# Performance work log

Hardware: AMD Instinct MI355X
Metric: run time of the kernel (lower is better)

Reference implementation:

```python
import jax, jax.numpy as jnp
import numpy as np

N = 50000      # nodes
E = 800000     # edges (avg degree 16)
IN = 512       # input_dim
R = 128        # feat_reduce_dim
F = 64         # hid_dim per head
H = 4          # n_heads
OUT = 64       # output_dim
ALPHA = 0.2    # leaky_relu slope


def setup_inputs() -> dict:
    key = jax.random.key(0)
    ks = jax.random.split(key, 12)
    x = jax.random.normal(ks[0], (N, IN), dtype=jnp.float32)
    edges = jax.random.randint(ks[1], (2, E), 0, N, dtype=jnp.int32)
    # per-head GAT layer params (fan-in scaled so exp(logits) stays finite)
    W_lin_h = jax.random.normal(ks[2], (H, R, IN), dtype=jnp.float32) * (IN ** -0.5)
    W_seq_h = jax.random.normal(ks[3], (H, F, R), dtype=jnp.float32) * (R ** -0.5)
    a1_h = jax.random.normal(ks[4], (H, F), dtype=jnp.float32) * (F ** -0.5)
    b1_h = jnp.zeros((H,), dtype=jnp.float32)
    a2_h = jax.random.normal(ks[5], (H, F), dtype=jnp.float32) * (F ** -0.5)
    b2_h = jnp.zeros((H,), dtype=jnp.float32)
    bias_h = jnp.zeros((H, F), dtype=jnp.float32)
    # classifier GAT layer (in = H*F = 256, out = OUT)
    W_lin_c = jax.random.normal(ks[6], (R, H * F), dtype=jnp.float32) * ((H * F) ** -0.5)
    W_seq_c = jax.random.normal(ks[7], (OUT, R), dtype=jnp.float32) * (R ** -0.5)
    a1_c = jax.random.normal(ks[8], (OUT,), dtype=jnp.float32) * (OUT ** -0.5)
    b1_c = jnp.zeros((), dtype=jnp.float32)
    a2_c = jax.random.normal(ks[9], (OUT,), dtype=jnp.float32) * (OUT ** -0.5)
    b2_c = jnp.zeros((), dtype=jnp.float32)
    bias_c = jnp.zeros((OUT,), dtype=jnp.float32)
    return dict(x=x, edges=edges, W_lin_h=W_lin_h, W_seq_h=W_seq_h, a1_h=a1_h,
                b1_h=b1_h, a2_h=a2_h, b2_h=b2_h, bias_h=bias_h,
                W_lin_c=W_lin_c, W_seq_c=W_seq_c, a1_c=a1_c, b1_c=b1_c,
                a2_c=a2_c, b2_c=b2_c, bias_c=bias_c)


def _gat_layer(x, src, dst, W_lin, W_seq, a1, b1, a2, b2, bias, concat):
    n = x.shape[0]
    h = x @ W_lin.T                    # [N, R]   (Linear, no bias)
    s = h @ W_seq.T                    # [N, F]   (Conv1d k=1 == matmul)
    f1 = s @ a1 + b1                   # [N]      (f_1 conv)
    f2 = s @ a2 + b2                   # [N]      (f_2 conv)
    logits = f1[src] + f2[dst]         # [E]  edge-gather
    coefs = jnp.exp(jax.nn.leaky_relu(logits, ALPHA))          # [E]
    denom = jax.ops.segment_sum(coefs, src, num_segments=n)    # [N]
    agg = jax.ops.segment_sum(coefs[:, None] * s[dst], src, num_segments=n)  # [N, F]
    ret = agg / denom[:, None] + bias
    return jax.nn.elu(ret) if concat else ret


def reference(x, edges, W_lin_h, W_seq_h, a1_h, b1_h, a2_h, b2_h, bias_h,
              W_lin_c, W_seq_c, a1_c, b1_c, a2_c, b2_c, bias_c):
    src, dst = edges[0], edges[1]
    # n_heads attention layers (concat=True), vmapped over the head axis
    heads = jax.vmap(
        lambda Wl, Ws, a1, b1, a2, b2, b: _gat_layer(
            x, src, dst, Wl, Ws, a1, b1, a2, b2, b, True)
    )(W_lin_h, W_seq_h, a1_h, b1_h, a2_h, b2_h, bias_h)        # [H, N, F]
    hcat = jnp.transpose(heads, (1, 0, 2)).reshape(x.shape[0], -1)  # [N, H*F]
    # classifier GAT layer (concat=False -> no ELU)
    out = _gat_layer(hcat, src, dst, W_lin_c, W_seq_c, a1_c, b1_c,
                     a2_c, b2_c, bias_c, False)                # [N, OUT]
    return out
```

## Files before the change

kernel.cpp:

```cpp
#include <hip/hip_runtime.h>
#include <hip/hip_bf16.h>
#include <cstddef>
#include <cstdint>

#define IN_DIM 512
#define R_DIM 128
#define F_DIM 64
#define H_NUM 4
#define OUT_DIM 64
#define HF 256

typedef __attribute__((ext_vector_type(4))) float f32x4;
typedef __attribute__((ext_vector_type(8))) short bf16x8;

typedef const __attribute__((address_space(1))) void gas_void;
typedef __attribute__((address_space(3))) void las_void;

__device__ __forceinline__ float bf2f(ushort u) {
    union { uint i; float f; } v; v.i = ((uint)u) << 16; return v.f;
}
__device__ __forceinline__ ushort f2bf(float f) {
    union { float f; uint i; } v; v.f = f;
    uint r = v.i + 0x7fff + ((v.i >> 16) & 1);
    return (ushort)(r >> 16);
}
__device__ __forceinline__ float u2f(uint u) {
    union { uint i; float f; } v; v.i = u; return v.f;
}

__global__ __launch_bounds__(256) void zero_i32(int* __restrict__ p, int n) {
    int i = blockIdx.x * 256 + threadIdx.x;
    if (i < n) p[i] = 0;
}

__global__ __launch_bounds__(256) void wcomb_kernel(const float* __restrict__ WlinH,
                                                    const float* __restrict__ WseqH,
                                                    const float* __restrict__ WlinC,
                                                    const float* __restrict__ WseqC,
                                                    ushort* __restrict__ Wc1,
                                                    ushort* __restrict__ Wc2) {
    int idx = blockIdx.x * 256 + threadIdx.x;
    if (idx < H_NUM * F_DIM * IN_DIM) {
        int i  = idx & (IN_DIM - 1);
        int hf = idx >> 9;
        int h  = hf >> 6;
        const float* ws = WseqH + (size_t)hf * R_DIM;
        const float* wl = WlinH + (size_t)h * R_DIM * IN_DIM + i;
        float acc = 0.0f;
#pragma unroll 8
        for (int r = 0; r < R_DIM; ++r) acc += ws[r] * wl[(size_t)r * IN_DIM];
        Wc1[idx] = f2bf(acc);
    } else {
        int idx2 = idx - H_NUM * F_DIM * IN_DIM;
        if (idx2 >= OUT_DIM * HF) return;
        int j = idx2 & (HF - 1);
        int o = idx2 >> 8;
        const float* ws = WseqC + (size_t)o * R_DIM;
        const float* wl = WlinC + j;
        float acc = 0.0f;
#pragma unroll 8
        for (int r = 0; r < R_DIM; ++r) acc += ws[r] * wl[(size_t)r * HF];
        Wc2[idx2] = f2bf(acc);
    }
}

template<int BN, int K, int FS>
__global__ __launch_bounds__(256) void gemm_f32a(const float* __restrict__ A,
                                                 const ushort* __restrict__ B,
                                                 ushort* __restrict__ C,
                                                 int M, int Ntot,
                                                 const float* __restrict__ a1,
                                                 const float* __restrict__ b1,
                                                 const float* __restrict__ a2,
                                                 const float* __restrict__ b2,
                                                 float* __restrict__ f1o,
                                                 float* __restrict__ f2o) {
    constexpr int NF = 4;
    __shared__ ushort As[32 * 64];
    __shared__ ushort Bs[BN * 64];
    const int tid = threadIdx.x;
    const int wave = tid >> 6;
    const int lane = tid & 63;
    const int lr = lane & 15;
    const int lg = lane >> 4;
    const int wr = wave & 1;
    const int wc = wave >> 1;

    const int b = blockIdx.x;
    const int by = (b >> 3) & 1;
    const int bx = (b >> 4) * 8 + (b & 7);
    const int nbx = (M + 31) >> 5;
    if (bx >= nbx) return;
    const int m0 = bx * 32;
    const int n0 = by * BN;
    const int h0 = by * 2;

    int base[2];
#pragma unroll
    for (int ks = 0; ks < 2; ++ks)
        base[ks] = lr * 128 + (((ks * 4 + lg) ^ (lr & 7)) * 16);
    const int abase0 = wr * 2048 + base[0];
    const int abase1 = wr * 2048 + base[1];

    const int s_row = tid >> 3;
    const int s_lchunk = tid & 7;
    int s_grow = m0 + s_row;
    if (s_grow >= M) s_grow = M - 1;
    const int s_ldsoff = s_row * 128 + ((s_lchunk ^ (s_row & 7)) * 16);
    const int s_goff = s_lchunk * 8;

    f32x4 acc[NF];
#pragma unroll
    for (int cb = 0; cb < NF; ++cb) acc[cb] = (f32x4)0.0f;

    for (int k0 = 0; k0 < K; k0 += 64) {
#pragma unroll
        for (int r = 0; r < BN / 32; ++r) {
            int off = r * 4096 + tid * 16;
            int row = off >> 7;
            int kch = ((off >> 4) & 7) ^ (row & 7);
            const ushort* g = B + (size_t)(n0 + row) * K + k0 + kch * 8;
            __builtin_amdgcn_global_load_lds((gas_void*)g,
                                             (las_void*)((char*)Bs + off), 16, 0, 0);
        }
        {
            const float* g = A + (size_t)s_grow * K + k0 + s_goff;
            float4 v0 = *(const float4*)(g);
            float4 v1 = *(const float4*)(g + 4);
            ushort us[8] = {f2bf(v0.x), f2bf(v0.y), f2bf(v0.z), f2bf(v0.w),
                            f2bf(v1.x), f2bf(v1.y), f2bf(v1.z), f2bf(v1.w)};
            *(uint4*)((char*)As + s_ldsoff) = *(const uint4*)us;
        }
        __syncthreads();
        {
            bf16x8 af0 = *(const bf16x8*)((const char*)As + abase0);
            bf16x8 af1 = *(const bf16x8*)((const char*)As + abase1);
            bf16x8 bfr[NF];
#pragma unroll
            for (int j = 0; j < NF; ++j)
                bfr[j] = *(const bf16x8*)((const char*)Bs + (wc * 4 + j) * 2048 + base[0]);
#pragma unroll
            for (int j = 0; j < NF; ++j)
                acc[j] = __builtin_amdgcn_mfma_f32_16x16x32_bf16(
                    af0, bfr[j], acc[j], 0, 0, 0);
#pragma unroll
            for (int j = 0; j < NF; ++j)
                bfr[j] = *(const bf16x8*)((const char*)Bs + (wc * 4 + j) * 2048 + base[1]);
#pragma unroll
            for (int j = 0; j < NF; ++j)
                acc[j] = __builtin_amdgcn_mfma_f32_16x16x32_bf16(
                    af1, bfr[j], acc[j], 0, 0, 0);
        }
        __syncthreads();
    }

    const int head = h0 + wc;
    float a1v[NF], a2v[NF];
#pragma unroll
    for (int cb = 0; cb < NF; ++cb) {
        int col = n0 + wc * 64 + cb * 16 + lr;
        a1v[cb] = a1[col];
        a2v[cb] = a2[col];
    }
    const int rowb = m0 + wr * 16 + lg * 4;
#pragma unroll
    for (int r = 0; r < 4; ++r) {
        int row = rowb + r;
        bool ok = row < M;
        float p1 = 0.f, p2 = 0.f;
#pragma unroll
        for (int cb = 0; cb < NF; ++cb) {
            float v = acc[cb][r];
            p1 += v * a1v[cb];
            p2 += v * a2v[cb];
            if (ok) C[(size_t)row * Ntot + n0 + wc * 64 + cb * 16 + lr] = f2bf(v);
        }
#pragma unroll
        for (int m = 1; m < 16; m <<= 1) {
            p1 += __shfl_xor(p1, m, 64);
            p2 += __shfl_xor(p2, m, 64);
        }
        if (lr == 0 && ok) {
            f1o[(size_t)row * FS + head] = p1 + b1[head];
            f2o[(size_t)row * FS + head] = p2 + b2[head];
        }
    }
}

template<int BN, int K, int FS>
__global__ __launch_bounds__(256) void gemm_bf16(const ushort* __restrict__ A,
                                                 const ushort* __restrict__ B,
                                                 ushort* __restrict__ C,
                                                 int M, int Ntot,
                                                 const float* __restrict__ a1,
                                                 const float* __restrict__ b1,
                                                 const float* __restrict__ a2,
                                                 const float* __restrict__ b2,
                                                 float* __restrict__ f1o,
                                                 float* __restrict__ f2o) {
    constexpr int NF = BN / 16;
    constexpr int HH = BN / 64;
    __shared__ ushort As[64 * 64];
    __shared__ ushort Bs[BN * 64];
    const int tid = threadIdx.x;
    const int wave = tid >> 6;
    const int lane = tid & 63;
    const int lr = lane & 15;
    const int lg = lane >> 4;
    const int m0 = blockIdx.x * 64;

    int base[2];
#pragma unroll
    for (int ks = 0; ks < 2; ++ks)
        base[ks] = lr * 128 + (((ks * 4 + lg) ^ (lr & 7)) * 16);
    const int abase0 = wave * 2048 + base[0];
    const int abase1 = wave * 2048 + base[1];

    f32x4 acc[NF];
#pragma unroll
    for (int cb = 0; cb < NF; ++cb) acc[cb] = (f32x4)0.0f;

    for (int k0 = 0; k0 < K; k0 += 64) {
#pragma unroll
        for (int r = 0; r < 2; ++r) {
            int off = r * 4096 + tid * 16;
            int row = off >> 7;
            int kch = ((off >> 4) & 7) ^ (row & 7);
            const ushort* g = A + (size_t)(m0 + row) * K + k0 + kch * 8;
            __builtin_amdgcn_global_load_lds((gas_void*)g,
                                             (las_void*)((char*)As + off), 16, 0, 0);
        }
#pragma unroll
        for (int r = 0; r < BN / 32; ++r) {
            int off = r * 4096 + tid * 16;
            int row = off >> 7;
            int kch = ((off >> 4) & 7) ^ (row & 7);
            const ushort* g = B + (size_t)row * K + k0 + kch * 8;
            __builtin_amdgcn_global_load_lds((gas_void*)g,
                                             (las_void*)((char*)Bs + off), 16, 0, 0);
        }
        __syncthreads();
        {
            bf16x8 af0 = *(const bf16x8*)((const char*)As + abase0);
            bf16x8 af1 = *(const bf16x8*)((const char*)As + abase1);
#pragma unroll
            for (int cg = 0; cg < NF / 4; ++cg) {
                bf16x8 bfr[4];
#pragma unroll
                for (int j = 0; j < 4; ++j)
                    bfr[j] = *(const bf16x8*)((const char*)Bs + (cg * 4 + j) * 2048 + base[0]);
#pragma unroll
                for (int j = 0; j < 4; ++j)
                    acc[cg * 4 + j] = __builtin_amdgcn_mfma_f32_16x16x32_bf16(
                        af0, bfr[j], acc[cg * 4 + j], 0, 0, 0);
#pragma unroll
                for (int j = 0; j < 4; ++j)
                    bfr[j] = *(const bf16x8*)((const char*)Bs + (cg * 4 + j) * 2048 + base[1]);
#pragma unroll
                for (int j = 0; j < 4; ++j)
                    acc[cg * 4 + j] = __builtin_amdgcn_mfma_f32_16x16x32_bf16(
                        af1, bfr[j], acc[cg * 4 + j], 0, 0, 0);
            }
        }
        __syncthreads();
    }

    float a1v[NF], a2v[NF];
#pragma unroll
    for (int cb = 0; cb < NF; ++cb) {
        int col = cb * 16 + lr;
        a1v[cb] = a1[col];
        a2v[cb] = a2[col];
    }
    const int rowb = m0 + wave * 16 + lg * 4;
#pragma unroll
    for (int r = 0; r < 4; ++r) {
        int row = rowb + r;
        bool ok = row < M;
#pragma unroll
        for (int hh = 0; hh < HH; ++hh) {
            float p1 = 0.f, p2 = 0.f;
#pragma unroll
            for (int c4 = 0; c4 < 4; ++c4) {
                int cb = hh * 4 + c4;
                float v = acc[cb][r];
                p1 += v * a1v[cb];
                p2 += v * a2v[cb];
                if (ok) C[(size_t)row * Ntot + cb * 16 + lr] = f2bf(v);
            }
#pragma unroll
            for (int m = 1; m < 16; m <<= 1) {
                p1 += __shfl_xor(p1, m, 64);
                p2 += __shfl_xor(p2, m, 64);
            }
            if (lr == 0 && ok) {
                f1o[(size_t)row * FS + hh] = p1 + b1[hh];
                f2o[(size_t)row * FS + hh] = p2 + b2[hh];
            }
        }
    }
}

__global__ __launch_bounds__(256) void hist_kernel(const int* __restrict__ src,
                                                   int* __restrict__ counts, int E) {
    int e = blockIdx.x * 256 + threadIdx.x;
    if (e < E) atomicAdd(&counts[src[e]], 1);
}

__global__ __launch_bounds__(256) void scan_blk(const int* __restrict__ counts,
                                                int* __restrict__ lexcl,
                                                int* __restrict__ part, int N) {
    __shared__ int wsum[4];
    int t = threadIdx.x;
    int g = blockIdx.x * 256 + t;
    int lane = t & 63, wid = t >> 6;
    int v = (g < N) ? counts[g] : 0;
    int x = v;
#pragma unroll
    for (int off = 1; off < 64; off <<= 1) {
        int u = __shfl_up(x, off, 64);
        if (lane >= off) x += u;
    }
    if (lane == 63) wsum[wid] = x;
    __syncthreads();
    int woff = 0;
#pragma unroll
    for (int w = 0; w < 3; ++w) if (w < wid) woff += wsum[w];
    int incl = x + woff;
    if (g < N) lexcl[g] = incl - v;
    if (t == 255) part[blockIdx.x] = incl;
}

__global__ __launch_bounds__(256) void scan_part(int* __restrict__ part, int nb) {
    __shared__ int wsum[4];
    int t = threadIdx.x;
    int lane = t & 63, wid = t >> 6;
    int v = (t < nb) ? part[t] : 0;
    int x = v;
#pragma unroll
    for (int off = 1; off < 64; off <<= 1) {
        int u = __shfl_up(x, off, 64);
        if (lane >= off) x += u;
    }
    if (lane == 63) wsum[wid] = x;
    __syncthreads();
    int woff = 0;
#pragma unroll
    for (int w = 0; w < 3; ++w) if (w < wid) woff += wsum[w];
    int incl = x + woff;
    __syncthreads();
    if (t < nb) part[t] = incl - v;
    if (t == 255) part[nb] = incl;
}

__global__ __launch_bounds__(256) void scan_add(const int* __restrict__ lexcl,
                                                const int* __restrict__ part,
                                                int* __restrict__ starts,
                                                int* __restrict__ cursor, int N, int nb) {
    int g = blockIdx.x * 256 + threadIdx.x;
    if (g < N) {
        int s = lexcl[g] + part[blockIdx.x];
        starts[g] = s;
        cursor[g] = s;
    }
    if (g == 0) starts[N] = part[nb];
}

__global__ __launch_bounds__(256) void scatter_kernel(const int* __restrict__ src,
                                                      const int* __restrict__ dst,
                                                      int* __restrict__ cursor,
                                                      int* __restrict__ dsts, int E) {
    int e = blockIdx.x * 256 + threadIdx.x;
    if (e >= E) return;
    int p = atomicAdd(&cursor[src[e]], 1);
    dsts[p] = dst[e];
}

__global__ __launch_bounds__(256) void gather1_kernel(const int* __restrict__ starts,
                                                      const int* __restrict__ dsts,
                                                      const float* __restrict__ f1,
                                                      const float* __restrict__ f2,
                                                      const ushort* __restrict__ S1,
                                                      const float* __restrict__ bias,
                                                      ushort* __restrict__ hcat, int N) {
    int n = (int)((blockIdx.x * blockDim.x + threadIdx.x) >> 6);
    int lane = threadIdx.x & 63;
    if (n >= N) return;
    const int es = lane >> 5;
    const int fl = lane & 31;
    const int head = fl >> 3;
    const float f1h = f1[(size_t)n * 4 + head];
    int beg = starts[n], end = starts[n + 1];
    float a[8] = {};
    float den = 0.f;
    int i = beg;

#define G1_EDGE(D)                                                            \
    {                                                                         \
        float g_ = f2[(size_t)(D) * 4 + head];                                \
        uint4 r_ = *(const uint4*)(S1 + (size_t)(D) * HF + fl * 8);           \
        float l_ = f1h + g_; l_ = l_ > 0.f ? l_ : 0.2f * l_;                  \
        float c_ = __expf(l_);                                                \
        a[0] += c_ * u2f(r_.x << 16);  a[1] += c_ * u2f(r_.x & 0xffff0000u);  \
        a[2] += c_ * u2f(r_.y << 16);  a[3] += c_ * u2f(r_.y & 0xffff0000u);  \
        a[4] += c_ * u2f(r_.z << 16);  a[5] += c_ * u2f(r_.z & 0xffff0000u);  \
        a[6] += c_ * u2f(r_.w << 16);  a[7] += c_ * u2f(r_.w & 0xffff0000u);  \
        den += c_;                                                            \
    }

    for (; i + 4 <= end; i += 4) {
        int dA = dsts[i + es];
        int dB = dsts[i + 2 + es];
        G1_EDGE(dA);
        G1_EDGE(dB);
    }
    if (i + 2 <= end) {
        int d = dsts[i + es];
        G1_EDGE(d);
        i += 2;
    }
    if (i < end && es == 0) {
        int d = dsts[i];
        G1_EDGE(d);
    }
#undef G1_EDGE

#pragma unroll
    for (int k = 0; k < 8; ++k) a[k] += __shfl_xor(a[k], 32, 64);
    den += __shfl_xor(den, 32, 64);

    if (es == 0) {
        float rd = __builtin_amdgcn_rcpf(den);
        float4 b0 = *(const float4*)(bias + fl * 8);
        float4 b1 = *(const float4*)(bias + fl * 8 + 4);
        float v[8];
        v[0] = a[0] * rd + b0.x; v[1] = a[1] * rd + b0.y;
        v[2] = a[2] * rd + b0.z; v[3] = a[3] * rd + b0.w;
        v[4] = a[4] * rd + b1.x; v[5] = a[5] * rd + b1.y;
        v[6] = a[6] * rd + b1.z; v[7] = a[7] * rd + b1.w;
        ushort us[8];
#pragma unroll
        for (int k = 0; k < 8; ++k) {
            float vv = v[k] > 0.f ? v[k] : __expf(v[k]) - 1.f;
            us[k] = f2bf(vv);
        }
        *(uint4*)(hcat + (size_t)n * HF + fl * 8) = *(const uint4*)us;
    }
}

__global__ __launch_bounds__(256) void gather2_kernel(const int* __restrict__ starts,
                                                      const int* __restrict__ dsts,
                                                      const float* __restrict__ f1,
                                                      const float* __restrict__ f2,
                                                      const ushort* __restrict__ S2,
                                                      const float* __restrict__ bias,
                                                      float* __restrict__ out, int N) {
    int n = (int)((blockIdx.x * blockDim.x + threadIdx.x) >> 6);
    int lane = threadIdx.x & 63;
    if (n >= N) return;
    const int es = lane >> 5;
    const int fl = lane & 31;
    const float f1u = f1[n];
    int beg = starts[n], end = starts[n + 1];
    float a0 = 0.f, a1 = 0.f, den = 0.f;
    int i = beg;

#define G2_EDGE(D)                                                            \
    {                                                                         \
        float g_ = f2[(D)];                                                   \
        uint r_ = *(const uint*)(S2 + (size_t)(D) * OUT_DIM + fl * 2);        \
        float l_ = f1u + g_; l_ = l_ > 0.f ? l_ : 0.2f * l_;                  \
        float c_ = __expf(l_);                                                \
        a0 += c_ * u2f(r_ << 16);                                             \
        a1 += c_ * u2f(r_ & 0xffff0000u);                                     \
        den += c_;                                                            \
    }

    for (; i + 4 <= end; i += 4) {
        int dA = dsts[i + es];
        int dB = dsts[i + 2 + es];
        G2_EDGE(dA);
        G2_EDGE(dB);
    }
    if (i + 2 <= end) {
        int d = dsts[i + es];
        G2_EDGE(d);
        i += 2;
    }
    if (i < end && es == 0) {
        int d = dsts[i];
        G2_EDGE(d);
    }
#undef G2_EDGE

    a0 += __shfl_xor(a0, 32, 64);
    a1 += __shfl_xor(a1, 32, 64);
    den += __shfl_xor(den, 32, 64);

    if (es == 0) {
        float rd = __builtin_amdgcn_rcpf(den);
        float2 b = *(const float2*)(bias + fl * 2);
        float2 o;
        o.x = a0 * rd + b.x;
        o.y = a1 * rd + b.y;
        *(float2*)(out + (size_t)n * OUT_DIM + fl * 2) = o;
    }
}

extern "C" void kernel_launch(void* const* d_in, const int* in_sizes, int n_in,
                              void* d_out, int out_size, void* d_ws, size_t ws_size,
                              hipStream_t stream) {
    const float* x      = (const float*)d_in[0];
    const int*   edges  = (const int*)d_in[1];
    const float* Wlin_h = (const float*)d_in[2];
    const float* Wseq_h = (const float*)d_in[3];
    const float* a1_h   = (const float*)d_in[4];
    const float* b1_h   = (const float*)d_in[5];
    const float* a2_h   = (const float*)d_in[6];
    const float* b2_h   = (const float*)d_in[7];
    const float* bias_h = (const float*)d_in[8];
    const float* Wlin_c = (const float*)d_in[9];
    const float* Wseq_c = (const float*)d_in[10];
    const float* a1_c   = (const float*)d_in[11];
    const float* b1_c   = (const float*)d_in[12];
    const float* a2_c   = (const float*)d_in[13];
    const float* b2_c   = (const float*)d_in[14];
    const float* bias_c = (const float*)d_in[15];

    const int N = in_sizes[0] / IN_DIM;
    const int E = in_sizes[1] / 2;
    const int* src = edges;
    const int* dst = edges + E;

    char* ws = (char*)d_ws;
    size_t off = 0;
    ushort* WC1   = (ushort*)(ws + off); off += (size_t)HF * IN_DIM * 2;
    ushort* WC2   = (ushort*)(ws + off); off += (size_t)OUT_DIM * HF * 2;
    ushort* S1    = (ushort*)(ws + off); off += (size_t)N * HF * 2;
    ushort* S2    = S1;
    ushort* HCAT  = (ushort*)(ws + off); off += (size_t)N * HF * 2;
    float*  F1    = (float*)(ws + off);  off += (size_t)N * H_NUM * 4;
    float*  F2    = (float*)(ws + off);  off += (size_t)N * H_NUM * 4;
    float*  F1c   = (float*)(ws + off);  off += (size_t)N * 4;
    float*  F2c   = (float*)(ws + off);  off += (size_t)N * 4;
    int* COUNTS   = (int*)(ws + off);    off += (size_t)N * 4;
    int* STARTS   = (int*)(ws + off);    off += ((size_t)N + 1) * 4;
    int* CURSOR   = (int*)(ws + off);    off += (size_t)N * 4;
    int* DSTS     = (int*)(ws + off);    off += (size_t)E * 4;
    int* LEXCL    = (int*)(ws + off);    off += (size_t)N * 4;
    int* PART     = (int*)(ws + off);    off += 512 * 4;

    float* out = (float*)d_out;

    const int eg = (E + 255) / 256;
    const int NB = (N + 255) / 256;

    hipLaunchKernelGGL(zero_i32, dim3(NB), dim3(256), 0, stream, COUNTS, N);
    hipLaunchKernelGGL(hist_kernel, dim3(eg), dim3(256), 0, stream, src, COUNTS, E);
    hipLaunchKernelGGL(scan_blk, dim3(NB), dim3(256), 0, stream, COUNTS, LEXCL, PART, N);
    hipLaunchKernelGGL(scan_part, dim3(1), dim3(256), 0, stream, PART, NB);
    hipLaunchKernelGGL(scan_add, dim3(NB), dim3(256), 0, stream, LEXCL, PART, STARTS, CURSOR, N, NB);
    hipLaunchKernelGGL(scatter_kernel, dim3(eg), dim3(256), 0, stream, src, dst, CURSOR, DSTS, E);

    hipLaunchKernelGGL(wcomb_kernel,
                       dim3((H_NUM * F_DIM * IN_DIM + OUT_DIM * HF + 255) / 256), dim3(256),
                       0, stream, Wlin_h, Wseq_h, Wlin_c, Wseq_c, WC1, WC2);

    {
        int nbx = (N + 31) / 32;
        int gx = 16 * ((nbx + 7) / 8);
        hipLaunchKernelGGL((gemm_f32a<128, IN_DIM, 4>), dim3(gx), dim3(256),
                           0, stream, x, WC1, S1, N, HF,
                           a1_h, b1_h, a2_h, b2_h, F1, F2);
    }

    hipLaunchKernelGGL(gather1_kernel, dim3((N + 3) / 4), dim3(256), 0, stream,
                       STARTS, DSTS, F1, F2, S1, bias_h, HCAT, N);

    hipLaunchKernelGGL((gemm_bf16<OUT_DIM, HF, 1>), dim3((N + 63) / 64, 1), dim3(256),
                       0, stream, HCAT, WC2, S2, N, OUT_DIM,
                       a1_c, b1_c, a2_c, b2_c, F1c, F2c);

    hipLaunchKernelGGL(gather2_kernel, dim3((N + 3) / 4), dim3(256), 0, stream,
                       STARTS, DSTS, F1c, F2c, S2, bias_c, out, N);
}
```

Baseline: 243.7 us.

## Split first-layer gather into feature slices with persistent grid-stride waves

The first-layer neighbor aggregation is reworked so each block handles one of 8 feature slices (32 features, half a head), and the grid is fixed at 1024 blocks whose waves stride over nodes, prefetching the next node's edge range. Each lane now reads 4 bytes per edge instead of 16, and four edges are processed in parallel per wave, using 16-lane groups. Each slice's blocks touch only a narrow column band of S1, aiming for better cache locality and load balance. The cost is that dsts and f2 are reread once per slice, there are more shuffle reductions, and per-lane loads are smaller.

Measured after the change: 492.6 us. +102.1%, slower.

```diff
diff --git a/kernel.cpp b/kernel.cpp
--- a/kernel.cpp
+++ b/kernel.cpp
@@ -376,75 +376,75 @@
     dsts[p] = dst[e];
 }
 
-__global__ __launch_bounds__(256) void gather1_kernel(const int* __restrict__ starts,
-                                                      const int* __restrict__ dsts,
-                                                      const float* __restrict__ f1,
-                                                      const float* __restrict__ f2,
-                                                      const ushort* __restrict__ S1,
-                                                      const float* __restrict__ bias,
-                                                      ushort* __restrict__ hcat, int N) {
-    int n = (int)((blockIdx.x * blockDim.x + threadIdx.x) >> 6);
-    int lane = threadIdx.x & 63;
+__global__ __launch_bounds__(256) void gather1s_kernel(const int* __restrict__ starts,
+                                                       const int* __restrict__ dsts,
+                                                       const float* __restrict__ f1,
+                                                       const float* __restrict__ f2,
+                                                       const ushort* __restrict__ S1,
+                                                       const float* __restrict__ bias,
+                                                       ushort* __restrict__ hcat, int N) {
+    const int b = blockIdx.x;
+    const int slice = b & 7;
+    const int j = b >> 3;
+    const int widx = threadIdx.x >> 6;
+    const int lane = threadIdx.x & 63;
+    const int es = lane >> 4;
+    const int fl = lane & 15;
+    const int head = slice >> 1;
+    const int fofs = slice * 32 + fl * 2;
+    const int WPS = (int)(gridDim.x >> 3) * 4;
+    const int wslot = j * 4 + widx;
+
+    const float2 bia = *(const float2*)(bias + fofs);
+
+    int n = wslot;
     if (n >= N) return;
-    const int es = lane >> 5;
-    const int fl = lane & 31;
-    const int head = fl >> 3;
-    const float f1h = f1[(size_t)n * 4 + head];
-    int beg = starts[n], end = starts[n + 1];
-    float a[8] = {};
-    float den = 0.f;
-    int i = beg;
-
-#define G1_EDGE(D)                                                            \
-    {                                                                         \
-        float g_ = f2[(size_t)(D) * 4 + head];                                \
-        uint4 r_ = *(const uint4*)(S1 + (size_t)(D) * HF + fl * 8);           \
-        float l_ = f1h + g_; l_ = l_ > 0.f ? l_ : 0.2f * l_;                  \
-        float c_ = __expf(l_);                                                \
-        a[0] += c_ * u2f(r_.x << 16);  a[1] += c_ * u2f(r_.x & 0xffff0000u);  \
-        a[2] += c_ * u2f(r_.y << 16);  a[3] += c_ * u2f(r_.y & 0xffff0000u);  \
-        a[4] += c_ * u2f(r_.z << 16);  a[5] += c_ * u2f(r_.z & 0xffff0000u);  \
-        a[6] += c_ * u2f(r_.w << 16);  a[7] += c_ * u2f(r_.w & 0xffff0000u);  \
-        den += c_;                                                            \
-    }
-
-    for (; i + 4 <= end; i += 4) {
-        int dA = dsts[i + es];
-        int dB = dsts[i + 2 + es];
-        G1_EDGE(dA);
-        G1_EDGE(dB);
-    }
-    if (i + 2 <= end) {
-        int d = dsts[i + es];
-        G1_EDGE(d);
-        i += 2;
-    }
-    if (i < end && es == 0) {
-        int d = dsts[i];
-        G1_EDGE(d);
-    }
-#undef G1_EDGE
-
-#pragma unroll
-    for (int k = 0; k < 8; ++k) a[k] += __shfl_xor(a[k], 32, 64);
-    den += __shfl_xor(den, 32, 64);
-
-    if (es == 0) {
-        float rd = __builtin_amdgcn_rcpf(den);
-        float4 b0 = *(const float4*)(bias + fl * 8);
-        float4 b1 = *(const float4*)(bias + fl * 8 + 4);
-        float v[8];
-        v[0] = a[0] * rd + b0.x; v[1] = a[1] * rd + b0.y;
-        v[2] = a[2] * rd + b0.z; v[3] = a[3] * rd + b0.w;
-        v[4] = a[4] * rd + b1.x; v[5] = a[5] * rd + b1.y;
-        v[6] = a[6] * rd + b1.z; v[7] = a[7] * rd + b1.w;
-        ushort us[8];
-#pragma unroll
-        for (int k = 0; k < 8; ++k) {
-            float vv = v[k] > 0.f ? v[k] : __expf(v[k]) - 1.f;
-            us[k] = f2bf(vv);
-        }
-        *(uint4*)(hcat + (size_t)n * HF + fl * 8) = *(const uint4*)us;
+    int beg = starts[n];
+    int end = starts[n + 1];
+    for (; n < N; ) {
+        int nn = n + WPS;
+        int nbeg = 0, nend = 0;
+        if (nn < N) {
+            nbeg = starts[nn];
+            nend = starts[nn + 1];
+        }
+        float f1h = f1[(size_t)n * 4 + head];
+        float a0 = 0.f, a1 = 0.f, den = 0.f;
+        int i = beg;
+        for (; i + 4 <= end; i += 4) {
+            int d = dsts[i + es];
+            float g = f2[(size_t)d * 4 + head];
+            uint r = *(const uint*)(S1 + (size_t)d * HF + fofs);
+            float l = f1h + g; l = l > 0.f ? l : 0.2f * l;
+            float c = __expf(l);
+            a0 += c * u2f(r << 16);
+            a1 += c * u2f(r & 0xffff0000u);
+            den += c;
+        }
+        if (i + es < end) {
+            int d = dsts[i + es];
+            float g = f2[(size_t)d * 4 + head];
+            uint r = *(const uint*)(S1 + (size_t)d * HF + fofs);
+            float l = f1h + g; l = l > 0.f ? l : 0.2f * l;
+            float c = __expf(l);
+            a0 += c * u2f(r << 16);
+            a1 += c * u2f(r & 0xffff0000u);
+            den += c;
+        }
+        a0 += __shfl_xor(a0, 16, 64);  a0 += __shfl_xor(a0, 32, 64);
+        a1 += __shfl_xor(a1, 16, 64);  a1 += __shfl_xor(a1, 32, 64);
+        den += __shfl_xor(den, 16, 64); den += __shfl_xor(den, 32, 64);
+        if (es == 0) {
+            float rd = __builtin_amdgcn_rcpf(den);
+            float v0 = a0 * rd + bia.x;
+            float v1 = a1 * rd + bia.y;
+            v0 = v0 > 0.f ? v0 : __expf(v0) - 1.f;
+            v1 = v1 > 0.f ? v1 : __expf(v1) - 1.f;
+            ushort2 o;
+            o.x = f2bf(v0); o.y = f2bf(v1);
+            *(ushort2*)(hcat + (size_t)n * HF + fofs) = o;
+        }
+        n = nn; beg = nbeg; end = nend;
     }
 }
 
@@ -574,7 +574,7 @@
                            a1_h, b1_h, a2_h, b2_h, F1, F2);
     }
 
-    hipLaunchKernelGGL(gather1_kernel, dim3((N + 3) / 4), dim3(256), 0, stream,
+    hipLaunchKernelGGL(gather1s_kernel, dim3(1024), dim3(256), 0, stream,
                        STARTS, DSTS, F1, F2, S1, bias_h, HCAT, N);
 
     hipLaunchKernelGGL((gemm_bf16<OUT_DIM, HF, 1>), dim3((N + 63) / 64, 1), dim3(256),
```
